# Kernel tuning notes

Measured on AMD Instinct MI355X. Metric: run time of the kernel, lower is better.

The kernel has to match this reference:

```python
import jax, jax.numpy as jnp
import numpy as np

C = 256
GN_GROUPS = 16
EPS = 1e-5


def hsigmoid(x):
    # HSigmoid(bias=3, divisor=6)
    return jnp.clip((x + 3.0) / 6.0, 0.0, 1.0)


def conv3x3(x, w, b):
    y = jax.lax.conv_general_dilated(x, w, (1, 1), ((1, 1), (1, 1)),
                                     dimension_numbers=('NCHW', 'OIHW', 'NCHW'))
    return y + b[None, :, None, None]


def group_norm(x, w, b):
    B, Cc, H, W = x.shape
    xg = x.reshape(B, GN_GROUPS, Cc // GN_GROUPS, H, W)
    mu = xg.mean(axis=(2, 3, 4), keepdims=True)
    var = xg.var(axis=(2, 3, 4), keepdims=True)
    xn = ((xg - mu) * jax.lax.rsqrt(var + EPS)).reshape(B, Cc, H, W)
    return xn * w[None, :, None, None] + b[None, :, None, None]


def bilinear_sample(x, py, px):
    # x: [B,C,H,W]; py,px: [B,9,Ho,Wo]; zero padding outside the image
    B, Cc, H, W = x.shape
    y0 = jnp.floor(py)
    x0 = jnp.floor(px)

    def gather(xb, yi, xi):
        return xb[:, yi, xi]  # [C,9,Ho,Wo]

    out = jnp.zeros((B, Cc) + py.shape[1:], x.dtype)
    for dy in (0.0, 1.0):
        for dx in (0.0, 1.0):
            yi = y0 + dy
            xi = x0 + dx
            wgt = (1.0 - jnp.abs(py - yi)) * (1.0 - jnp.abs(px - xi))
            valid = (yi >= 0) & (yi <= H - 1) & (xi >= 0) & (xi <= W - 1)
            yc = jnp.clip(yi, 0, H - 1).astype(jnp.int32)
            xc = jnp.clip(xi, 0, W - 1).astype(jnp.int32)
            vals = jax.vmap(gather)(x, yc, xc)  # [B,C,9,Ho,Wo]
            out = out + vals * (wgt * valid)[:, None]
    return out


def mdcn(x, offset, mask, w, stride):
    # Modulated deformable conv v2, kernel 3x3, padding 1, no bias.
    B, Cin, H, W = x.shape
    Ho, Wo = offset.shape[2], offset.shape[3]
    off = offset.reshape(B, 9, 2, Ho, Wo)  # channel 2k = y_k, 2k+1 = x_k
    kk = jnp.arange(9)
    ky = (kk // 3).astype(x.dtype)[None, :, None, None]
    kx = (kk % 3).astype(x.dtype)[None, :, None, None]
    gy = (jnp.arange(Ho, dtype=x.dtype) * stride - 1.0)[None, None, :, None]
    gx = (jnp.arange(Wo, dtype=x.dtype) * stride - 1.0)[None, None, None, :]
    py = gy + ky + off[:, :, 0]
    px = gx + kx + off[:, :, 1]
    cols = bilinear_sample(x, py, px) * mask[:, None]  # [B,Cin,9,Ho,Wo]
    return jnp.einsum('bckhw,ock->bohw', cols, w.reshape(w.shape[0], Cin, 9))


def resize_bilinear_ac(x, oh, ow):
    # F.interpolate(mode='bilinear', align_corners=True), separable
    B, Cc, H, W = x.shape
    ys = jnp.linspace(0.0, H - 1.0, oh)
    y0 = jnp.floor(ys).astype(jnp.int32)
    y1 = jnp.minimum(y0 + 1, H - 1)
    wy = (ys - y0)[None, None, :, None]
    xr = x[:, :, y0, :] * (1 - wy) + x[:, :, y1, :] * wy
    xs = jnp.linspace(0.0, W - 1.0, ow)
    x0i = jnp.floor(xs).astype(jnp.int32)
    x1i = jnp.minimum(x0i + 1, W - 1)
    wx = (xs - x0i)[None, None, None, :]
    return xr[:, :, :, x0i] * (1 - wx) + xr[:, :, :, x1i] * wx


def dyrelu(x, w1, b1, w2, b2):
    p = x.mean(axis=(2, 3))  # [B,C] global avg pool
    h = jax.nn.relu(p @ w1.reshape(w1.shape[0], -1).T + b1)
    co = hsigmoid(h @ w2.reshape(w2.shape[0], -1).T + b2) - 0.5  # [B,4C]
    a1, c1, a2, c2 = jnp.split(co, 4, axis=1)
    a1 = (a1 * 2.0 + 1.0)[:, :, None, None]
    a2 = (a2 * 2.0)[:, :, None, None]
    c1 = c1[:, :, None, None]
    c2 = c2[:, :, None, None]
    return jnp.maximum(x * a1 + c1, x * a2 + c2)


def dyhead_block(xs, w_off, b_off, w_high, gn_high_w, gn_high_b,
                 w_mid, gn_mid_w, gn_mid_b, w_low, gn_low_w, gn_low_b,
                 sa_w, sa_b, dy_w1, dy_b1, dy_w2, dy_b2):
    def scale_attn(f):
        p = f.mean(axis=(2, 3))  # [B,C]
        v = hsigmoid(jax.nn.relu(p @ sa_w.reshape(1, -1).T + sa_b))
        return v[:, :, None, None]  # [B,1,1,1]

    outs = []
    n = len(xs)
    for lvl in range(n):
        om = conv3x3(xs[lvl], w_off, b_off)
        offset = om[:, :18]
        mask = jax.nn.sigmoid(om[:, 18:])
        mid = group_norm(mdcn(xs[lvl], offset, mask, w_mid, 1), gn_mid_w, gn_mid_b)
        s = mid * scale_attn(mid)
        cnt = 1.0
        if lvl > 0:
            lo = group_norm(mdcn(xs[lvl - 1], offset, mask, w_low, 2),
                            gn_low_w, gn_low_b)
            s = s + lo * scale_attn(lo)
            cnt += 1.0
        if lvl < n - 1:
            # so take the stride-2 subgrid (clean interpretation of mmdet code)
            hi = group_norm(mdcn(xs[lvl + 1], offset[:, :, ::2, ::2],
                                 mask[:, :, ::2, ::2], w_high, 1),
                            gn_high_w, gn_high_b)
            hi = resize_bilinear_ac(hi, xs[lvl].shape[2], xs[lvl].shape[3])
            s = s + hi * scale_attn(hi)
            cnt += 1.0
        outs.append(dyrelu(s / cnt, dy_w1, dy_b1, dy_w2, dy_b2))
    return tuple(outs)


def setup_inputs() -> dict:
    key = jax.random.key(0)
    ks = jax.random.split(key, 10)
    B = 4
    sizes = [(64, 64), (32, 32), (16, 16)]
    inp = {}
    for i, (h, w) in enumerate(sizes):
        inp[f'x{i}'] = jax.random.normal(ks[i], (B, C, h, w), jnp.float32)
    std = 0.01  # normal_init(m, 0, 0.01)
    inp['w_off'] = jax.random.normal(ks[3], (27, C, 3, 3), jnp.float32) * std
    inp['b_off'] = jnp.zeros((27,), jnp.float32)
    inp['w_high'] = jax.random.normal(ks[4], (C, C, 3, 3), jnp.float32) * std
    inp['w_mid'] = jax.random.normal(ks[5], (C, C, 3, 3), jnp.float32) * std
    inp['w_low'] = jax.random.normal(ks[6], (C, C, 3, 3), jnp.float32) * std
    for nm in ('high', 'mid', 'low'):
        inp[f'gn_{nm}_w'] = jnp.ones((C,), jnp.float32)
        inp[f'gn_{nm}_b'] = jnp.zeros((C,), jnp.float32)
    inp['sa_w'] = jax.random.normal(ks[7], (1, C, 1, 1), jnp.float32) * std
    inp['sa_b'] = jnp.zeros((1,), jnp.float32)
    inp['dy_w1'] = jax.random.normal(ks[8], (C // 4, C, 1, 1), jnp.float32) * std
    inp['dy_b1'] = jnp.zeros((C // 4,), jnp.float32)
    inp['dy_w2'] = jax.random.normal(ks[9], (4 * C, C // 4, 1, 1), jnp.float32) * std
    inp['dy_b2'] = jnp.zeros((4 * C,), jnp.float32)
    return inp


def reference(x0, x1, x2, w_off, b_off, w_high, gn_high_w, gn_high_b,
              w_mid, gn_mid_w, gn_mid_b, w_low, gn_low_w, gn_low_b,
              sa_w, sa_b, dy_w1, dy_b1, dy_w2, dy_b2):
    return dyhead_block([x0, x1, x2], w_off, b_off, w_high, gn_high_w, gn_high_b,
                        w_mid, gn_mid_w, gn_mid_b, w_low, gn_low_w, gn_low_b,
                        sa_w, sa_b, dy_w1, dy_b1, dy_w2, dy_b2)
```

## Files before the change

### kernel.cpp

```cpp
#include <hip/hip_runtime.h>
#include <math.h>

#define CH 256
#define GRP 16
#define EPSV 1e-5f
#define BB 4

typedef __attribute__((ext_vector_type(8))) short short8;
typedef __attribute__((ext_vector_type(4))) short short4v;
typedef __attribute__((ext_vector_type(4))) float f32x4;

__device__ __forceinline__ float hsig(float x){
  return fminf(fmaxf((x + 3.0f) * (1.0f/6.0f), 0.0f), 1.0f);
}

__device__ __forceinline__ unsigned short f2bf(float f){
  union { float f; unsigned int u; } v; v.f = f;
  unsigned int r = v.u + 0x7fffu + ((v.u >> 16) & 1u);
  return (unsigned short)(r >> 16);
}

__device__ __forceinline__ float bf2f(unsigned short u){
  union { float f; unsigned int i; } v; v.i = ((unsigned int)u) << 16; return v.f;
}

__device__ __forceinline__ void gload_lds16(const void* g, void* l){
  __builtin_amdgcn_global_load_lds((const __attribute__((address_space(1))) unsigned int*)g,
                                   (__attribute__((address_space(3))) unsigned int*)l, 16, 0, 0);
}

__global__ __launch_bounds__(256) void prep_kernel(
    const float* __restrict__ w_mid, const float* __restrict__ w_low, const float* __restrict__ w_high,
    const float* __restrict__ w_off,
    const float* __restrict__ x0, const float* __restrict__ x1, const float* __restrict__ x2,
    unsigned short* __restrict__ Wm, unsigned short* __restrict__ Wl, unsigned short* __restrict__ Wh,
    unsigned short* __restrict__ W27,
    float* __restrict__ xn0, float* __restrict__ xn1, float* __restrict__ xn2,
    float* __restrict__ roww0, float* __restrict__ roww1){
  __shared__ float lds[32][257];
  int blk = blockIdx.x;
  int t = threadIdx.x;
  if (blk < 6912){
    const float* w = (blk < 2304) ? w_mid : (blk < 4608 ? w_low : w_high);
    unsigned short* W3 = (blk < 2304) ? Wm : (blk < 4608 ? Wl : Wh);
    int idx = (blk % 2304) * 256 + t;
    int e = idx & 7;
    int l = (idx >> 3) & 63;
    int f = idx >> 9;
    int mf = f & 3;
    int q = (f >> 2) & 3;
    int s = f >> 4;
    int kk = s >> 3, cb = s & 7;
    int o = q * 64 + mf * 16 + (l & 15);
    int kc = ((l >> 4) << 3) + e;
    int c = cb * 32 + kc;
    W3[idx] = f2bf(w[(o * CH + c) * 9 + kk]);
    return;
  }
  if (blk < 7200){
    int idx = (blk - 6912) * 256 + t;
    int s = idx >> 10;
    int r = idx & 1023;
    int o = r >> 5;
    int pos = r & 31;
    int cp = pos >> 3, j = pos & 7;
    int kc = ((cp ^ ((o >> 1) & 3)) << 3) + j;
    int kk = s >> 3, cb = s & 7;
    int c = (cb << 5) + kc;
    W27[idx] = (o < 27) ? f2bf(w_off[(o * CH + c) * 9 + kk]) : (unsigned short)0;
    return;
  }
  if (blk >= 7872){
    float* out = (blk == 7873) ? roww1 : roww0;
    int Hh = (blk == 7873) ? 16 : 32;
    int H = (blk == 7873) ? 32 : 64;
    if (t < Hh){
      float rs = 0.0f;
      float scale = (float)(Hh - 1) / (float)(H - 1);
      for (int h = 0; h < H; h++){
        float ysv = (float)h * scale;
        float y0f = floorf(ysv);
        int y0 = (int)y0f;
        float fy = ysv - y0f;
        int y1 = min(y0 + 1, Hh - 1);
        if (y0 == t) rs += 1.0f - fy;
        if (y1 == t) rs += fy;
      }
      out[t] = rs;
    }
    return;
  }
  int nb = blk - 7200;
  const float* xs; float* xd; int HW; int rb;
  if (nb < 512){ xs = x0; xd = xn0; HW = 4096; rb = nb; }
  else if (nb < 640){ xs = x1; xd = xn1; HW = 1024; rb = nb - 512; }
  else { xs = x2; xd = xn2; HW = 256; rb = nb - 640; }
  int p0 = rb * 32;
  int b = p0 / HW;
  int rem0 = p0 - b * HW;
  int pl = t & 31, cg = t >> 5;
  for (int ci = 0; ci < 32; ci++){
    int c = ci * 8 + cg;
    lds[pl][c] = xs[(long)(b * CH + c) * HW + rem0 + pl];
  }
  __syncthreads();
  for (int p = 0; p < 32; p++){
    xd[(long)(b * HW + rem0 + p) * CH + t] = lds[p][t];
  }
}

__global__ __launch_bounds__(256, 4) void conv_offset_mfma_kernel(
    const float* __restrict__ xn0, const float* __restrict__ xn1, const float* __restrict__ xn2,
    const unsigned short* __restrict__ W27, const float* __restrict__ boff,
    float* __restrict__ offs_all, float* __restrict__ mask_all){
  __shared__ __align__(16) short awlds[1024];
  __shared__ __align__(16) short cbuf[4096];
  int blk = blockIdx.x;
  const float* xn; int H; long ooff, moff; int rb;
  if (blk < 256){ xn = xn0; H = 64; ooff = 0; moff = 0; rb = blk; }
  else if (blk < 320){ xn = xn1; H = 32; ooff = 294912; moff = 147456; rb = blk - 256; }
  else { xn = xn2; H = 16; ooff = 368640; moff = 184320; rb = blk - 320; }
  int W = H, HW = H * W;
  int t = threadIdx.x;
  int lane = t & 63, wv = t >> 6;
  int pxp = t >> 2, cgp = t & 3;
  int pg = rb * 64 + pxp;
  int b = pg / HW;
  int rem = pg - b * HW;
  int i = rem / W, j = rem - i * W;

  f32x4 acc[2];
  #pragma unroll
  for (int mf = 0; mf < 2; mf++){
    #pragma unroll
    for (int r = 0; r < 4; r++){
      int o = mf * 16 + (lane >> 4) * 4 + r;
      acc[mf][r] = boff[o < 27 ? o : 0];
    }
  }

  for (int kk = 0; kk < 9; kk++){
    int ky = kk / 3, kx = kk - ky * 3;
    int ii = i - 1 + ky, jj = j - 1 + kx;
    bool valid = (ii >= 0 && ii < H && jj >= 0 && jj < W);
    int addr = valid ? ((b * HW + ii * W + jj) << 8) : 0;
    float vm = valid ? 1.0f : 0.0f;
    for (int cb8 = 0; cb8 < 8; cb8++){
      __syncthreads();
      const unsigned short* tile = W27 + (size_t)(kk * 8 + cb8) * 1024;
      if (t < 128) gload_lds16(tile + (t >> 6) * 512 + (t & 63) * 8, (short*)awlds + (t >> 6) * 512);
      const float* xc = xn + addr + cb8 * 32 + cgp * 8;
      float4 va = *(const float4*)xc;
      float4 vb = *(const float4*)(xc + 4);
      short8 pk;
      pk[0] = (short)f2bf(vm * va.x); pk[1] = (short)f2bf(vm * va.y);
      pk[2] = (short)f2bf(vm * va.z); pk[3] = (short)f2bf(vm * va.w);
      pk[4] = (short)f2bf(vm * vb.x); pk[5] = (short)f2bf(vm * vb.y);
      pk[6] = (short)f2bf(vm * vb.z); pk[7] = (short)f2bf(vm * vb.w);
      *(short8*)((char*)cbuf + pxp * 64 + ((cgp ^ ((pxp >> 1) & 3)) << 4)) = pk;
      __syncthreads();
      short8 af[2];
      #pragma unroll
      for (int mf = 0; mf < 2; mf++){
        int o = mf * 16 + (lane & 15);
        af[mf] = *(const short8*)((const char*)awlds + o * 64 + ((((lane >> 4)) ^ ((o >> 1) & 3)) << 4));
      }
      int nc = wv * 16 + (lane & 15);
      short8 bf1 = *(const short8*)((const char*)cbuf + nc * 64 + ((((lane >> 4)) ^ ((nc >> 1) & 3)) << 4));
      acc[0] = __builtin_amdgcn_mfma_f32_16x16x32_bf16(af[0], bf1, acc[0], 0, 0, 0);
      acc[1] = __builtin_amdgcn_mfma_f32_16x16x32_bf16(af[1], bf1, acc[1], 0, 0, 0);
    }
  }

  int rem0 = rb * 64 - b * HW;
  #pragma unroll
  for (int mf = 0; mf < 2; mf++){
    #pragma unroll
    for (int r = 0; r < 4; r++){
      int o = mf * 16 + (lane >> 4) * 4 + r;
      int pix = rem0 + wv * 16 + (lane & 15);
      float v = acc[mf][r];
      if (o < 18) offs_all[ooff + ((long)b * 18 + o) * HW + pix] = v;
      else if (o < 27) mask_all[moff + ((long)b * 9 + (o - 18)) * HW + pix] = 1.0f / (1.0f + expf(-v));
    }
  }
}

__device__ const int MJ_start[8] = {0,128,160,168,200,208,240,248};
__device__ const int MJ_xsel[7]  = {0,1,2,0,1,1,2};
__device__ const int MJ_Hx[7]    = {64,32,16,64,32,32,16};
__device__ const int MJ_ooff[7]  = {0,294912,368640,294912,368640,0,294912};
__device__ const int MJ_moff[7]  = {0,147456,184320,147456,184320,0,147456};
__device__ const int MJ_Hoff[7]  = {64,32,16,32,16,64,32};
__device__ const int MJ_ostep[7] = {1,1,1,1,1,2,2};
__device__ const int MJ_strd[7]  = {1,1,1,2,2,1,1};
__device__ const int MJ_wsel[7]  = {0,0,0,1,1,2,2};
__device__ const int MJ_yoff[7]  = {0,5242880,7602176,6291456,7864320,4194304,7340032};
__device__ const int MJ_Ho[7]    = {64,32,16,32,16,32,16};

__global__ __launch_bounds__(512, 2) void mdcn_mfma_kernel(
    const float* __restrict__ xn0, const float* __restrict__ xn1, const float* __restrict__ xn2,
    const float* __restrict__ offs_all, const float* __restrict__ mask_all,
    const unsigned short* __restrict__ Wm, const unsigned short* __restrict__ Wl, const unsigned short* __restrict__ Wh,
    unsigned short* __restrict__ y_all){
  __shared__ __align__(16) short colbuf[4][4096];

  int dd = (blockIdx.x & 7) * 31 + (blockIdx.x >> 3);
  int job = 0;
  while (job < 6 && dd >= MJ_start[job + 1]) job++;
  int xsel = MJ_xsel[job];
  const float* xn = (xsel == 0) ? xn0 : (xsel == 1 ? xn1 : xn2);
  int wsel = MJ_wsel[job];
  const unsigned short* W3 = (wsel == 0) ? Wm : (wsel == 1 ? Wl : Wh);
  int Hx = MJ_Hx[job], Wx = Hx, HxWx = Hx * Hx;
  int Ho = MJ_Ho[job], Wo = Ho, HoWo = Ho * Ho;
  int Woff = MJ_Hoff[job], HoffW = Woff * Woff;
  int ostep = MJ_ostep[job], stride = MJ_strd[job];
  const float* offs = offs_all + MJ_ooff[job];
  const float* maskb = mask_all + MJ_moff[job];
  unsigned short* y = y_all + MJ_yoff[job];

  int rb = dd - MJ_start[job];
  int blkPerB = HoWo >> 7;
  int b = rb / blkPerB;
  int n0 = (rb - b * blkPerB) << 7;

  int t = threadIdx.x;
  int lane = t & 63;
  int wv = t >> 6;
  int wq = wv >> 1;
  int px = t >> 2;
  int cg = t & 3;

  int pix = n0 + px;
  int i = pix / Wo, j = pix - i * Wo;
  int opos = i * ostep * Woff + j * ostep;
  int base = b * HxWx;

  int4 A4c, A4n; float4 Wtc, Wtn;
  auto computeAW = [&](int kk, int4& A4o, float4& Wto){
    int ky = kk / 3, kx = kk - ky * 3;
    float offy = offs[((long)b * 18 + 2 * kk) * HoffW + opos];
    float offx = offs[((long)b * 18 + 2 * kk + 1) * HoffW + opos];
    float m = maskb[((long)b * 9 + kk) * HoffW + opos];
    float py = (float)(i * stride - 1 + ky) + offy;
    float pxx = (float)(j * stride - 1 + kx) + offx;
    float y0f = floorf(py), x0f = floorf(pxx);
    float fy = py - y0f, fx = pxx - x0f;
    bool vy0 = (y0f >= 0.0f) && (y0f <= (float)(Hx - 1));
    bool vy1 = (y0f + 1.0f >= 0.0f) && (y0f + 1.0f <= (float)(Hx - 1));
    bool vx0 = (x0f >= 0.0f) && (x0f <= (float)(Wx - 1));
    bool vx1 = (x0f + 1.0f >= 0.0f) && (x0f + 1.0f <= (float)(Wx - 1));
    float w0 = (1.0f - fy) * (1.0f - fx) * m * ((vy0 && vx0) ? 1.0f : 0.0f);
    float w1 = (1.0f - fy) * fx * m * ((vy0 && vx1) ? 1.0f : 0.0f);
    float w2 = fy * (1.0f - fx) * m * ((vy1 && vx0) ? 1.0f : 0.0f);
    float w3 = fy * fx * m * ((vy1 && vx1) ? 1.0f : 0.0f);
    int iy0 = min(max((int)y0f, 0), Hx - 1);
    int iy1 = min(max((int)y0f + 1, 0), Hx - 1);
    int ix0 = min(max((int)x0f, 0), Wx - 1);
    int ix1 = min(max((int)x0f + 1, 0), Wx - 1);
    A4o = make_int4((base + iy0 * Wx + ix0) << 8, (base + iy0 * Wx + ix1) << 8,
                    (base + iy1 * Wx + ix0) << 8, (base + iy1 * Wx + ix1) << 8);
    Wto = make_float4(w0, w1, w2, w3);
  };

  float4 g0_0,g0_1,g0_2,g0_3,g0_4,g0_5,g0_6,g0_7;
  float4 g1_0,g1_1,g1_2,g1_3,g1_4,g1_5,g1_6,g1_7;

  short8 af0[4], af1[4];
  auto loadA = [&](int s, short8* af){
    const short8* wp = (const short8*)W3 + ((size_t)s * 16 + wq * 4) * 64 + lane;
    af[0] = wp[0]; af[1] = wp[64]; af[2] = wp[128]; af[3] = wp[192];
  };

  f32x4 acc[4][4];
  #pragma unroll
  for (int mf = 0; mf < 4; mf++)
    #pragma unroll
    for (int nf = 0; nf < 4; nf++)
      acc[mf][nf] = (f32x4){0.f, 0.f, 0.f, 0.f};

#define GATHER_(P, CB, A4G) do{ \
    const float* xc_ = xn + (CB)*32 + cg*8; \
    g##P##_0 = *(const float4*)(xc_ + (A4G).x); g##P##_1 = *(const float4*)(xc_ + (A4G).x + 4); \
    g##P##_2 = *(const float4*)(xc_ + (A4G).y); g##P##_3 = *(const float4*)(xc_ + (A4G).y + 4); \
    g##P##_4 = *(const float4*)(xc_ + (A4G).z); g##P##_5 = *(const float4*)(xc_ + (A4G).z + 4); \
    g##P##_6 = *(const float4*)(xc_ + (A4G).w); g##P##_7 = *(const float4*)(xc_ + (A4G).w + 4); \
  }while(0)

#define PACKW_(P, BUF, WT) do{ \
    short8 pk_; \
    pk_[0] = (short)f2bf((WT).x*g##P##_0.x + (WT).y*g##P##_2.x + (WT).z*g##P##_4.x + (WT).w*g##P##_6.x); \
    pk_[1] = (short)f2bf((WT).x*g##P##_0.y + (WT).y*g##P##_2.y + (WT).z*g##P##_4.y + (WT).w*g##P##_6.y); \
    pk_[2] = (short)f2bf((WT).x*g##P##_0.z + (WT).y*g##P##_2.z + (WT).z*g##P##_4.z + (WT).w*g##P##_6.z); \
    pk_[3] = (short)f2bf((WT).x*g##P##_0.w + (WT).y*g##P##_2.w + (WT).z*g##P##_4.w + (WT).w*g##P##_6.w); \
    pk_[4] = (short)f2bf((WT).x*g##P##_1.x + (WT).y*g##P##_3.x + (WT).z*g##P##_5.x + (WT).w*g##P##_7.x); \
    pk_[5] = (short)f2bf((WT).x*g##P##_1.y + (WT).y*g##P##_3.y + (WT).z*g##P##_5.y + (WT).w*g##P##_7.y); \
    pk_[6] = (short)f2bf((WT).x*g##P##_1.z + (WT).y*g##P##_3.z + (WT).z*g##P##_5.z + (WT).w*g##P##_7.z); \
    pk_[7] = (short)f2bf((WT).x*g##P##_1.w + (WT).y*g##P##_3.w + (WT).z*g##P##_5.w + (WT).w*g##P##_7.w); \
    *(short8*)((char*)colbuf[BUF] + px * 64 + ((cg ^ ((px >> 1) & 3)) << 4)) = pk_; \
  }while(0)

#define MFMA_(BUF, AF) do{ \
    __builtin_amdgcn_s_setprio(1); \
    short8 bf_[4]; \
    _Pragma("unroll") \
    for (int nf = 0; nf < 4; nf++){ \
      int nc_ = (wv & 1) * 64 + nf * 16 + (lane & 15); \
      bf_[nf] = *(const short8*)((const char*)colbuf[BUF] + nc_ * 64 + ((((lane >> 4)) ^ ((nc_ >> 1) & 3)) << 4)); } \
    _Pragma("unroll") \
    for (int mf = 0; mf < 4; mf++) \
      _Pragma("unroll") \
      for (int nf = 0; nf < 4; nf++) \
        acc[mf][nf] = __builtin_amdgcn_mfma_f32_16x16x32_bf16((AF)[mf], bf_[nf], acc[mf][nf], 0, 0, 0); \
    __builtin_amdgcn_s_setprio(0); \
  }while(0)

#define BARRIER_ do{ \
    asm volatile("s_waitcnt lgkmcnt(0)" ::: "memory"); \
    __builtin_amdgcn_sched_barrier(0); \
    __builtin_amdgcn_s_barrier(); \
    __builtin_amdgcn_sched_barrier(0); \
  }while(0)

#define PHASE_(P, PC, PN) do{ \
    if ((P) <= 34){ PACKW_(0, (PN), Wtc); PACKW_(1, (PN)+1, Wtc); } \
    if ((P) <= 33){ \
      if (((2*(P)+4) & 7) == 0){ \
        computeAW((2*(P)+4) >> 3, A4n, Wtn); \
        GATHER_(0, 0, A4n); \
        GATHER_(1, 1, A4n); \
      } else { \
        GATHER_(0, (2*(P)+4) & 7, A4c); \
        GATHER_(1, (2*(P)+5) & 7, A4c); \
      } \
    } \
    MFMA_((PC), af0); \
    MFMA_((PC)+1, af1); \
    if ((P) <= 34){ loadA(2*(P)+2, af0); loadA(2*(P)+3, af1); } \
    if ((P) <= 33 && ((2*(P)+4) & 7) == 0){ A4c = A4n; Wtc = Wtn; } \
    BARRIER_; \
  }while(0)

  computeAW(0, A4c, Wtc);
  loadA(0, af0);
  loadA(1, af1);
  GATHER_(0, 0, A4c);
  GATHER_(1, 1, A4c);
  PACKW_(0, 0, Wtc);
  PACKW_(1, 1, Wtc);
  GATHER_(0, 2, A4c);
  GATHER_(1, 3, A4c);
  BARRIER_;

  for (int pp = 0; pp < 36; pp += 2){
    PHASE_(pp, 0, 2);
    PHASE_(pp + 1, 2, 0);
  }

#undef PHASE_
#undef BARRIER_
#undef MFMA_
#undef PACKW_
#undef GATHER_

  #pragma unroll
  for (int mf = 0; mf < 4; mf++){
    #pragma unroll
    for (int nf = 0; nf < 4; nf++){
      #pragma unroll
      for (int r = 0; r < 4; r++){
        int o = wq * 64 + mf * 16 + (lane >> 4) * 4 + r;
        int pix2 = n0 + (wv & 1) * 64 + nf * 16 + (lane & 15);
        y[((long)b * CH + o) * HoWo + pix2] = f2bf(acc[mf][nf][r]);
      }
    }
  }
}

__device__ const int SJ_yoff[7] = {0,4194304,5242880,6291456,7340032,7602176,7864320};
__device__ const int SJ_HW[7]   = {4096,1024,1024,1024,256,256,256};
__device__ const int SJ_rw[7]   = {0,1,0,0,2,0,0};

__global__ __launch_bounds__(256) void stats_all_kernel(
    const unsigned short* __restrict__ y_all, const float* __restrict__ roww0, const float* __restrict__ roww1,
    float* __restrict__ sums_all, float* __restrict__ ss_all, float* __restrict__ wsum_all){
  int blk = blockIdx.x;
  int job = blk >> 10, bc = blk & 1023;
  int HW = SJ_HW[job];
  int Ws = (HW == 4096) ? 64 : ((HW == 1024) ? 32 : 16);
  int rwsel = SJ_rw[job];
  const float* rw = (rwsel == 2) ? roww1 : roww0;
  const unsigned short* p = y_all + SJ_yoff[job] + (long)bc * HW;
  int t = threadIdx.x;
  float s = 0, ss = 0, ws = 0;
  for (int e0 = t * 8; e0 < HW; e0 += 2048){
    short8 v8 = *(const short8*)(p + e0);
    float vv[8];
    #pragma unroll
    for (int jj = 0; jj < 8; jj++) vv[jj] = bf2f((unsigned short)v8[jj]);
    #pragma unroll
    for (int jj = 0; jj < 8; jj++){ s += vv[jj]; ss += vv[jj] * vv[jj]; }
    if (rwsel){
      int r = e0 / Ws, cc = e0 - r * Ws;
      float rr = rw[r];
      float rsum = 0;
      #pragma unroll
      for (int jj = 0; jj < 8; jj++) rsum += vv[jj] * rw[cc + jj];
      ws += rr * rsum;
    }
  }
  __shared__ float r1[256], r2[256], r3[256];
  r1[t] = s; r2[t] = ss; r3[t] = ws;
  __syncthreads();
  for (int o = 128; o > 0; o >>= 1){
    if (t < o){ r1[t] += r1[t + o]; r2[t] += r2[t + o]; r3[t] += r3[t + o]; }
    __syncthreads();
  }
  if (t == 0){
    sums_all[job * 1024 + bc] = r1[0];
    ss_all[job * 1024 + bc] = r2[0];
    if (rwsel) wsum_all[(rwsel - 1) * 1024 + bc] = r3[0];
  }
}

__device__ const int   GJ_psrc[7] = {0,1,0,0,2,0,0};
__device__ const float GJ_pdiv[7] = {1.f/4096,1.f/4096,1.f/1024,1.f/1024,1.f/1024,1.f/256,1.f/256};
__device__ const float GJ_ninv[7] = {1.f/65536,1.f/16384,1.f/16384,1.f/16384,1.f/4096,1.f/4096,1.f/4096};
__device__ const int   GJ_gsel[7] = {0,2,0,1,2,0,1};

__global__ __launch_bounds__(256) void gn_sa_all_kernel(
    const float* __restrict__ sums_all, const float* __restrict__ ss_all, const float* __restrict__ wsum_all,
    const float* __restrict__ gw_m, const float* __restrict__ gb_m,
    const float* __restrict__ gw_l, const float* __restrict__ gb_l,
    const float* __restrict__ gw_h, const float* __restrict__ gb_h,
    const float* __restrict__ saw, const float* __restrict__ sab,
    float* __restrict__ mu_all, float* __restrict__ rs_all, float* __restrict__ v_all){
  int blk = blockIdx.x;
  int job = blk >> 2, b = blk & 3;
  int t = threadIdx.x;
  const float* sums = sums_all + job * 1024;
  const float* ssq  = ss_all + job * 1024;
  int psrc = GJ_psrc[job];
  const float* ps = (psrc == 0) ? sums : (wsum_all + (psrc - 1) * 1024);
  int gsel = GJ_gsel[job];
  const float* gw = (gsel == 0) ? gw_m : (gsel == 1 ? gw_l : gw_h);
  const float* gb = (gsel == 0) ? gb_m : (gsel == 1 ? gb_l : gb_h);
  float pdiv = GJ_pdiv[job], ninv = GJ_ninv[job];
  __shared__ float smu[GRP], srs[GRP], red[256];
  if (t < GRP){
    float s = 0, ss = 0;
    for (int c = 0; c < 16; c++){ int idx = b * CH + t * 16 + c; s += sums[idx]; ss += ssq[idx]; }
    float mu = s * ninv;
    float var = ss * ninv - mu * mu;
    float rs = rsqrtf(var + EPSV);
    smu[t] = mu; srs[t] = rs;
    mu_all[job * 64 + b * GRP + t] = mu;
    rs_all[job * 64 + b * GRP + t] = rs;
  }
  __syncthreads();
  int g = t >> 4;
  float pm = (ps[b * CH + t] * pdiv - smu[g]) * srs[g] * gw[t] + gb[t];
  red[t] = pm * saw[t];
  __syncthreads();
  for (int o = 128; o > 0; o >>= 1){ if (t < o) red[t] += red[t + o]; __syncthreads(); }
  if (t == 0) v_all[job * 4 + b] = hsig(fmaxf(red[0] + sab[0], 0.0f));
}

__device__ const long CA_yb[3] = {0, 5242880, 7602176};
__device__ const long CA_yl[3] = {0, 6291456, 7864320};
__device__ const long CA_yh[3] = {4194304, 7340032, 0};
__device__ const int  CA_ms[3] = {0, 2, 5};
__device__ const int  CA_ls[3] = {0, 3, 6};
__device__ const int  CA_hs[3] = {1, 4, 0};
__device__ const long FA_out[3] = {0, 4194304, 5242880};

__global__ __launch_bounds__(256) void dyrelu_direct_kernel(
    const float* __restrict__ sums_all, const float* __restrict__ wsum_all,
    const float* __restrict__ mu_all, const float* __restrict__ rs_all, const float* __restrict__ v_all,
    const float* __restrict__ gw_m, const float* __restrict__ gb_m,
    const float* __restrict__ gw_l, const float* __restrict__ gb_l,
    const float* __restrict__ gw_h, const float* __restrict__ gb_h,
    const float* __restrict__ w1, const float* __restrict__ b1,
    const float* __restrict__ w2, const float* __restrict__ b2,
    float* __restrict__ coef_all){
  int lvl = blockIdx.x >> 2, b = blockIdx.x & 3;
  int t = threadIdx.x;
  int H = 64 >> lvl, HW = H * H;
  float invHW = 1.0f / (float)HW;
  int has_lo = (lvl > 0), has_hi = (lvl < 2);
  float inv_cnt = 1.0f / (1.0f + has_lo + has_hi);
  int ms = CA_ms[lvl], ls = CA_ls[lvl], hs = CA_hs[lvl];
  int g = t >> 4;
  float p = v_all[ms * 4 + b] *
      ((sums_all[ms * 1024 + b * CH + t] * invHW - mu_all[ms * 64 + b * GRP + g]) * rs_all[ms * 64 + b * GRP + g] * gw_m[t] + gb_m[t]);
  if (has_lo)
    p += v_all[ls * 4 + b] *
      ((sums_all[ls * 1024 + b * CH + t] * invHW - mu_all[ls * 64 + b * GRP + g]) * rs_all[ls * 64 + b * GRP + g] * gw_l[t] + gb_l[t]);
  if (has_hi)
    p += v_all[hs * 4 + b] *
      ((wsum_all[lvl * 1024 + b * CH + t] * invHW - mu_all[hs * 64 + b * GRP + g]) * rs_all[hs * 64 + b * GRP + g] * gw_h[t] + gb_h[t]);
  p *= inv_cnt;
  __shared__ float pl[CH], hl[64];
  pl[t] = p;
  __syncthreads();
  if (t < 64){
    float a = b1[t];
    const float* wr = w1 + t * CH;
    for (int c = 0; c < CH; c++) a += wr[c] * pl[c];
    hl[t] = fmaxf(a, 0.0f);
  }
  __syncthreads();
  #pragma unroll
  for (int r = 0; r < 4; r++){
    int o = r * CH + t;
    float a = b2[o];
    const float* wr = w2 + o * 64;
    #pragma unroll
    for (int j = 0; j < 64; j++) a += wr[j] * hl[j];
    float co = hsig(a) - 0.5f;
    float outv;
    if (r == 0) outv = co * 2.0f + 1.0f;
    else if (r == 2) outv = co * 2.0f;
    else outv = co;
    coef_all[lvl * 4096 + (b * 4 + r) * CH + t] = outv;
  }
}

__global__ __launch_bounds__(256) void combine_final_kernel(
    const unsigned short* __restrict__ y_all,
    const float* __restrict__ mu_all, const float* __restrict__ rs_all, const float* __restrict__ v_all,
    const float* __restrict__ gw_m, const float* __restrict__ gb_m,
    const float* __restrict__ gw_l, const float* __restrict__ gb_l,
    const float* __restrict__ gw_h, const float* __restrict__ gb_h,
    const float* __restrict__ coef_all, float* __restrict__ outp){
  int blk = blockIdx.x;
  int lvl, rb;
  if (blk < 4096){ lvl = 0; rb = blk; }
  else if (blk < 5120){ lvl = 1; rb = blk - 4096; }
  else { lvl = 2; rb = blk - 5120; }
  int H = 64 >> lvl, W = H, HW = H * W;
  int has_lo = (lvl > 0), has_hi = (lvl < 2);
  float inv_cnt = 1.0f / (1.0f + has_lo + has_hi);
  int ms = CA_ms[lvl], ls = CA_ls[lvl], hs = CA_hs[lvl];
  const unsigned short* smid = y_all + CA_yb[lvl];
  const unsigned short* ylo = y_all + CA_yl[lvl];
  const unsigned short* yhi = y_all + CA_yh[lvl];

  int t = threadIdx.x;
  int idx = (rb * 256 + t) * 4;
  int b = idx / (CH * HW);
  int r1i = idx - b * CH * HW;
  int c = r1i / HW;
  int rem = r1i - c * HW;
  int h = rem / W;
  int w = rem - h * W;
  int g = c >> 4;
  int bg = b * GRP + g;

  short4v m4 = *(const short4v*)(smid + idx);
  float vms = v_all[ms * 4 + b], mum = mu_all[ms * 64 + bg], rsm = rs_all[ms * 64 + bg];
  float gm = gw_m[c], bm = gb_m[c];
  float4 s4;
  s4.x = vms * ((bf2f((unsigned short)m4[0]) - mum) * rsm * gm + bm);
  s4.y = vms * ((bf2f((unsigned short)m4[1]) - mum) * rsm * gm + bm);
  s4.z = vms * ((bf2f((unsigned short)m4[2]) - mum) * rsm * gm + bm);
  s4.w = vms * ((bf2f((unsigned short)m4[3]) - mum) * rsm * gm + bm);
  if (has_lo){
    short4v l4 = *(const short4v*)(ylo + idx);
    float vls = v_all[ls * 4 + b], mul = mu_all[ls * 64 + bg], rsl = rs_all[ls * 64 + bg];
    float gl = gw_l[c], bl = gb_l[c];
    s4.x += vls * ((bf2f((unsigned short)l4[0]) - mul) * rsl * gl + bl);
    s4.y += vls * ((bf2f((unsigned short)l4[1]) - mul) * rsl * gl + bl);
    s4.z += vls * ((bf2f((unsigned short)l4[2]) - mul) * rsl * gl + bl);
    s4.w += vls * ((bf2f((unsigned short)l4[3]) - mul) * rsl * gl + bl);
  }
  if (has_hi){
    int Hh = H >> 1, Wh = W >> 1;
    float ysv = (float)h * ((float)(Hh - 1) / (float)(H - 1));
    float y0f = floorf(ysv); int y0 = (int)y0f; float fy = ysv - y0f; int y1 = min(y0 + 1, Hh - 1);
    const unsigned short* hb = yhi + (long)(b * CH + c) * Hh * Wh;
    float vhs = v_all[hs * 4 + b], muh = mu_all[hs * 64 + bg], rsh = rs_all[hs * 64 + bg];
    float gh = gw_h[c], bh = gb_h[c];
    float xscale = (float)(Wh - 1) / (float)(W - 1);
    float* sp = (float*)&s4;
    #pragma unroll
    for (int dw = 0; dw < 4; dw++){
      float xsv = (float)(w + dw) * xscale;
      float x0f = floorf(xsv); int x0 = (int)x0f; float fx = xsv - x0f; int x1 = min(x0 + 1, Wh - 1);
      float v00 = bf2f(hb[y0 * Wh + x0]), v01 = bf2f(hb[y0 * Wh + x1]);
      float v10 = bf2f(hb[y1 * Wh + x0]), v11 = bf2f(hb[y1 * Wh + x1]);
      float blv = v00 * (1 - fy) * (1 - fx) + v01 * (1 - fy) * fx + v10 * fy * (1 - fx) + v11 * fy * fx;
      sp[dw] += vhs * ((blv - muh) * rsh * gh + bh);
    }
  }
  const float* cf = coef_all + lvl * 4096 + b * 4 * CH;
  float a1 = cf[c], c1 = cf[CH + c], a2 = cf[2 * CH + c], c2 = cf[3 * CH + c];
  float4 o4;
  float sx = s4.x * inv_cnt, sy = s4.y * inv_cnt, sz = s4.z * inv_cnt, sw = s4.w * inv_cnt;
  o4.x = fmaxf(sx * a1 + c1, sx * a2 + c2);
  o4.y = fmaxf(sy * a1 + c1, sy * a2 + c2);
  o4.z = fmaxf(sz * a1 + c1, sz * a2 + c2);
  o4.w = fmaxf(sw * a1 + c1, sw * a2 + c2);
  *(float4*)(outp + FA_out[lvl] + idx) = o4;
}

extern "C" void kernel_launch(void* const* d_in, const int* in_sizes, int n_in,
                              void* d_out, int out_size, void* d_ws, size_t ws_size,
                              hipStream_t stream){
  const float* x0 = (const float*)d_in[0];
  const float* x1 = (const float*)d_in[1];
  const float* x2 = (const float*)d_in[2];
  const float* w_off = (const float*)d_in[3];
  const float* b_off = (const float*)d_in[4];
  int sig = (in_sizes[6] == 256);
  const float* w_high = (const float*)d_in[5];
  const float* w_mid  = (const float*)d_in[sig ? 8 : 6];
  const float* w_low  = (const float*)d_in[sig ? 11 : 7];
  const float* gn_high_w = (const float*)d_in[sig ? 6 : 8];
  const float* gn_high_b = (const float*)d_in[sig ? 7 : 9];
  const float* gn_mid_w  = (const float*)d_in[sig ? 9 : 10];
  const float* gn_mid_b  = (const float*)d_in[sig ? 10 : 11];
  const float* gn_low_w  = (const float*)d_in[12];
  const float* gn_low_b  = (const float*)d_in[13];
  const float* sa_w  = (const float*)d_in[14];
  const float* sa_b  = (const float*)d_in[15];
  const float* dy_w1 = (const float*)d_in[16];
  const float* dy_b1 = (const float*)d_in[17];
  const float* dy_w2 = (const float*)d_in[18];
  const float* dy_b2 = (const float*)d_in[19];

  float* p = (float*)d_ws;
  unsigned short* W3_mid  = (unsigned short*)p; p += 294912;
  unsigned short* W3_low  = (unsigned short*)p; p += 294912;
  unsigned short* W3_high = (unsigned short*)p; p += 294912;
  unsigned short* W27     = (unsigned short*)p; p += 36864;
  float* xn0 = p; p += 4194304;
  float* xn1 = p; p += 1048576;
  float* xn2 = p; p += 262144;
  float* offs_all = p; p += 387072;
  float* mask_all = p; p += 193536;
  unsigned short* y_all = (unsigned short*)p; p += 4063232;
  float* sums_all = p; p += 7168;
  float* ss_all = p; p += 7168;
  float* wsum_all = p; p += 2048;
  float* coef_all = p; p += 12288;
  float* mu_all = p; p += 448;
  float* rs_all = p; p += 448;
  float* v_all = p; p += 28;   p += 4;
  float* roww0 = p; p += 32;
  float* roww1 = p; p += 32;

  prep_kernel<<<7874, 256, 0, stream>>>(w_mid, w_low, w_high, w_off, x0, x1, x2,
                                        W3_mid, W3_low, W3_high, W27,
                                        xn0, xn1, xn2, roww0, roww1);
  conv_offset_mfma_kernel<<<336, 256, 0, stream>>>(xn0, xn1, xn2, W27, b_off, offs_all, mask_all);
  mdcn_mfma_kernel<<<248, 512, 0, stream>>>(xn0, xn1, xn2, offs_all, mask_all, W3_mid, W3_low, W3_high, y_all);
  stats_all_kernel<<<7168, 256, 0, stream>>>(y_all, roww0, roww1, sums_all, ss_all, wsum_all);
  gn_sa_all_kernel<<<28, 256, 0, stream>>>(sums_all, ss_all, wsum_all,
                                           gn_mid_w, gn_mid_b, gn_low_w, gn_low_b, gn_high_w, gn_high_b,
                                           sa_w, sa_b, mu_all, rs_all, v_all);
  dyrelu_direct_kernel<<<12, 256, 0, stream>>>(sums_all, wsum_all, mu_all, rs_all, v_all,
                                               gn_mid_w, gn_mid_b, gn_low_w, gn_low_b, gn_high_w, gn_high_b,
                                               dy_w1, dy_b1, dy_w2, dy_b2, coef_all);
  combine_final_kernel<<<5376, 256, 0, stream>>>(y_all, mu_all, rs_all, v_all,
                                                 gn_mid_w, gn_mid_b, gn_low_w, gn_low_b, gn_high_w, gn_high_b,
                                                 coef_all, (float*)d_out);
}
```

Baseline: 195.9 us.

## Fuse per-channel statistics into MDCN epilogue, replace stats pass with tiny reducer

```diff
diff --git a/kernel.cpp b/kernel.cpp
--- a/kernel.cpp
+++ b/kernel.cpp
@@ -202,8 +202,10 @@
     const float* __restrict__ xn0, const float* __restrict__ xn1, const float* __restrict__ xn2,
     const float* __restrict__ offs_all, const float* __restrict__ mask_all,
     const unsigned short* __restrict__ Wm, const unsigned short* __restrict__ Wl, const unsigned short* __restrict__ Wh,
-    unsigned short* __restrict__ y_all){
+    const float* __restrict__ roww0, const float* __restrict__ roww1,
+    unsigned short* __restrict__ y_all, float* __restrict__ gpart){
   __shared__ __align__(16) short colbuf[4][4096];
+  __shared__ float pstat[2][256][3];
 
   int dd = (blockIdx.x & 7) * 31 + (blockIdx.x >> 3);
   int job = 0;
@@ -364,64 +366,73 @@
 #undef PACKW_
 #undef GATHER_
 
+  const float* rw = (job == 5) ? roww0 : ((job == 6) ? roww1 : (const float*)nullptr);
+  int woLog = (Wo == 64) ? 6 : ((Wo == 32) ? 5 : 4);
+  int nhalf = wv & 1;
   #pragma unroll
   for (int mf = 0; mf < 4; mf++){
     #pragma unroll
-    for (int nf = 0; nf < 4; nf++){
+    for (int r = 0; r < 4; r++){
+      int o = wq * 64 + mf * 16 + (lane >> 4) * 4 + r;
+      float s = 0.0f, ss = 0.0f, ws = 0.0f;
       #pragma unroll
-      for (int r = 0; r < 4; r++){
-        int o = wq * 64 + mf * 16 + (lane >> 4) * 4 + r;
-        int pix2 = n0 + (wv & 1) * 64 + nf * 16 + (lane & 15);
-        y[((long)b * CH + o) * HoWo + pix2] = f2bf(acc[mf][nf][r]);
+      for (int nf = 0; nf < 4; nf++){
+        int pix2 = n0 + nhalf * 64 + nf * 16 + (lane & 15);
+        unsigned short ub = f2bf(acc[mf][nf][r]);
+        y[((long)b * CH + o) * HoWo + pix2] = ub;
+        float vq = bf2f(ub);
+        s += vq; ss += vq * vq;
+        if (rw){
+          int i2 = pix2 >> woLog, j2 = pix2 & (Wo - 1);
+          ws += vq * rw[i2] * rw[j2];
+        }
+      }
+      #pragma unroll
+      for (int m2 = 1; m2 < 16; m2 <<= 1){
+        s  += __shfl_xor(s, m2, 64);
+        ss += __shfl_xor(ss, m2, 64);
+        if (rw) ws += __shfl_xor(ws, m2, 64);
+      }
+      if ((lane & 15) == 0){
+        pstat[nhalf][o][0] = s;
+        pstat[nhalf][o][1] = ss;
+        pstat[nhalf][o][2] = rw ? ws : 0.0f;
       }
     }
   }
-}
-
-__device__ const int SJ_yoff[7] = {0,4194304,5242880,6291456,7340032,7602176,7864320};
-__device__ const int SJ_HW[7]   = {4096,1024,1024,1024,256,256,256};
-__device__ const int SJ_rw[7]   = {0,1,0,0,2,0,0};
-
-__global__ __launch_bounds__(256) void stats_all_kernel(
-    const unsigned short* __restrict__ y_all, const float* __restrict__ roww0, const float* __restrict__ roww1,
+  __syncthreads();
+  if (t < 256){
+    float s  = pstat[0][t][0] + pstat[1][t][0];
+    float ss = pstat[0][t][1] + pstat[1][t][1];
+    float ws = pstat[0][t][2] + pstat[1][t][2];
+    float* gp = gpart + (size_t)dd * 768 + t * 3;
+    gp[0] = s; gp[1] = ss; gp[2] = ws;
+  }
+}
+
+__device__ const int SR_mj[7]      = {0, 5, 1, 3, 6, 2, 4};
+__device__ const int SR_tilesPB[7] = {32, 8, 8, 8, 2, 2, 2};
+
+__global__ __launch_bounds__(256) void stats_reduce_kernel(
+    const float* __restrict__ gpart,
     float* __restrict__ sums_all, float* __restrict__ ss_all, float* __restrict__ wsum_all){
-  int blk = blockIdx.x;
-  int job = blk >> 10, bc = blk & 1023;
-  int HW = SJ_HW[job];
-  int Ws = (HW == 4096) ? 64 : ((HW == 1024) ? 32 : 16);
-  int rwsel = SJ_rw[job];
-  const float* rw = (rwsel == 2) ? roww1 : roww0;
-  const unsigned short* p = y_all + SJ_yoff[job] + (long)bc * HW;
-  int t = threadIdx.x;
-  float s = 0, ss = 0, ws = 0;
-  for (int e0 = t * 8; e0 < HW; e0 += 2048){
-    short8 v8 = *(const short8*)(p + e0);
-    float vv[8];
-    #pragma unroll
-    for (int jj = 0; jj < 8; jj++) vv[jj] = bf2f((unsigned short)v8[jj]);
-    #pragma unroll
-    for (int jj = 0; jj < 8; jj++){ s += vv[jj]; ss += vv[jj] * vv[jj]; }
-    if (rwsel){
-      int r = e0 / Ws, cc = e0 - r * Ws;
-      float rr = rw[r];
-      float rsum = 0;
-      #pragma unroll
-      for (int jj = 0; jj < 8; jj++) rsum += vv[jj] * rw[cc + jj];
-      ws += rr * rsum;
-    }
-  }
-  __shared__ float r1[256], r2[256], r3[256];
-  r1[t] = s; r2[t] = ss; r3[t] = ws;
-  __syncthreads();
-  for (int o = 128; o > 0; o >>= 1){
-    if (t < o){ r1[t] += r1[t + o]; r2[t] += r2[t + o]; r3[t] += r3[t + o]; }
-    __syncthreads();
-  }
-  if (t == 0){
-    sums_all[job * 1024 + bc] = r1[0];
-    ss_all[job * 1024 + bc] = r2[0];
-    if (rwsel) wsum_all[(rwsel - 1) * 1024 + bc] = r3[0];
-  }
+  int tid = blockIdx.x * 256 + threadIdx.x;
+  int sj = tid >> 10;
+  int rem = tid & 1023;
+  int b = rem >> 8;
+  int c = rem & 255;
+  int mj = SR_mj[sj];
+  int tiles = SR_tilesPB[sj];
+  int dd0 = MJ_start[mj] + b * tiles;
+  float s = 0.0f, ss = 0.0f, ws = 0.0f;
+  for (int ti = 0; ti < tiles; ti++){
+    const float* gp = gpart + (size_t)(dd0 + ti) * 768 + c * 3;
+    s += gp[0]; ss += gp[1]; ws += gp[2];
+  }
+  sums_all[sj * 1024 + rem] = s;
+  ss_all[sj * 1024 + rem] = ss;
+  if (sj == 1) wsum_all[rem] = ws;
+  else if (sj == 4) wsum_all[1024 + rem] = ws;
 }
 
 __device__ const int   GJ_psrc[7] = {0,1,0,0,2,0,0};
@@ -641,6 +652,7 @@
   float* offs_all = p; p += 387072;
   float* mask_all = p; p += 193536;
   unsigned short* y_all = (unsigned short*)p; p += 4063232;
+  float* gpart = p; p += 190464;
   float* sums_all = p; p += 7168;
   float* ss_all = p; p += 7168;
   float* wsum_all = p; p += 2048;
@@ -655,8 +667,9 @@
                                         W3_mid, W3_low, W3_high, W27,
                                         xn0, xn1, xn2, roww0, roww1);
   conv_offset_mfma_kernel<<<336, 256, 0, stream>>>(xn0, xn1, xn2, W27, b_off, offs_all, mask_all);
-  mdcn_mfma_kernel<<<248, 512, 0, stream>>>(xn0, xn1, xn2, offs_all, mask_all, W3_mid, W3_low, W3_high, y_all);
-  stats_all_kernel<<<7168, 256, 0, stream>>>(y_all, roww0, roww1, sums_all, ss_all, wsum_all);
+  mdcn_mfma_kernel<<<248, 512, 0, stream>>>(xn0, xn1, xn2, offs_all, mask_all,
+                                            W3_mid, W3_low, W3_high, roww0, roww1, y_all, gpart);
+  stats_reduce_kernel<<<28, 256, 0, stream>>>(gpart, sums_all, ss_all, wsum_all);
   gn_sa_all_kernel<<<28, 256, 0, stream>>>(sums_all, ss_all, wsum_all,
                                            gn_mid_w, gn_mid_b, gn_low_w, gn_low_b, gn_high_w, gn_high_b,
                                            sa_w, sa_b, mu_all, rs_all, v_all);
```

Result: slower. 202.0 us (+3.1%).
